# Kernel optimization log

Hardware: AMD Instinct MI355X
Metric: run time of the kernel (lower is better)

## Reference

```python
import jax, jax.numpy as jnp
import numpy as np

B, L, D = 32, 128, 512
Qn = 16          # n_querys
N, P = 512, 64   # gathered groups x group size


def setup_inputs() -> dict:
    key = jax.random.key(0)
    ks = jax.random.split(key, 10)
    s = 0.02
    return {
        "patch": jax.random.normal(ks[0], (B, L, D), jnp.float32),
        "query": jax.random.normal(ks[1], (1, Qn, D), jnp.float32),
        "Wk": jax.random.normal(ks[2], (D, D), jnp.float32) * s,
        "bk": jnp.zeros((D,), jnp.float32),
        "Wv": jax.random.normal(ks[3], (D, D), jnp.float32) * s,
        "bv": jnp.zeros((D,), jnp.float32),
        "Wf": jax.random.normal(ks[4], (D, 1), jnp.float32) * s,
        "bf": jnp.zeros((1,), jnp.float32),
        "indices": jax.random.randint(ks[5], (N, P), 0, B * L),
        "pos_mask": jax.random.bernoulli(ks[6], 0.8, (N, P)),
    }


def reference(patch, query, Wk, bk, Wv, bv, Wf, bf, indices, pos_mask):
    # patch: [B,L,D]; query: [1,q,D]; indices: [N,P] into B*L; pos_mask: [N,P]
    b, l, d = patch.shape
    q = query.shape[1]
    scale = 1.0 / jnp.sqrt(jnp.asarray(d, patch.dtype))
    Q0 = query[0]                                   # [q,D]
    # Projections (proj_k/proj_v applied to [Q ; patch]); Q row identical across batch
    KQ = Q0 @ Wk + bk                               # [q,D]
    Kp = patch @ Wk + bk                            # [B,L,D]
    VQ = Q0 @ Wv + bv                               # [q,D]
    Vp = patch @ Wv + bv                            # [B,L,D]
    # attn scores: self-token column (same for every batch) + patch columns
    s_self = jnp.einsum('qd,qd->q', Q0, KQ) * scale            # [q]
    s_patch = jnp.einsum('qd,bld->blq', Q0, Kp) * scale        # [B,L,q]
    # gather groups of tokens by flat index
    g = s_patch.reshape(b * l, q)[indices]                     # [N,P,q]
    g = jnp.where(pos_mask[:, :, None], g, -jnp.inf)
    g = jnp.transpose(g, (0, 2, 1))                            # [N,q,P]
    scores = jnp.concatenate(
        [jnp.broadcast_to(s_self[None, :, None], (g.shape[0], q, 1)), g], axis=-1)
    w = jax.nn.softmax(scores, axis=-1)                        # [N,q,P+1]
    # gathered values (value of a token is independent of q in the original)
    Vg = Vp.reshape(b * l, d)[indices]                         # [N,P,D]
    Vg = jnp.where(pos_mask[:, :, None], Vg, 0.0)
    patch_token = w[:, :, 0:1] * VQ[None] \
        + jnp.einsum('nqp,npd->nqd', w[:, :, 1:], Vg)          # [N,q,D]
    # fusion attention pooling over the q query axis
    fw = jax.nn.softmax(jnp.einsum('nqd,do->nqo', patch_token, Wf) + bf, axis=1)
    return jnp.sum(patch_token * fw, axis=1)                   # [N,D]
```

## Files before the change

kernel.cpp:

```cpp
#include <hip/hip_runtime.h>
#include <hip/hip_bf16.h>
#include <math.h>

#define DD    512
#define QN    16
#define NTOK  4096
#define MEXT  4112
#define MPAD  4224
#define NGRP  512
#define PP    64
#define NB    576
#define SCALE 0.04419417382415922f

typedef __bf16 bf16x8 __attribute__((ext_vector_type(8)));
typedef float  f32x4  __attribute__((ext_vector_type(4)));

static __device__ __forceinline__ ushort f2bf(float f) {
    __hip_bfloat16 h = __float2bfloat16(f);
    return *reinterpret_cast<ushort*>(&h);
}
static __device__ __forceinline__ float2 bfp2f2(unsigned int v) {
    float2 r;
    r.x = __uint_as_float(v << 16);
    r.y = __uint_as_float(v & 0xffff0000u);
    return r;
}
static __device__ __forceinline__ void gload16(const void* g, void* l) {
    __builtin_amdgcn_global_load_lds(
        (const __attribute__((address_space(1))) void*)g,
        (__attribute__((address_space(3))) void*)l, 16, 0, 0);
}

__global__ __launch_bounds__(256) void pack_all(
    const float* __restrict__ patch, const float* __restrict__ query,
    const float* __restrict__ Wv, const float* __restrict__ Wk,
    const float* __restrict__ bk,
    ushort* __restrict__ Xb, ushort* __restrict__ Bb, float* __restrict__ c0)
{
    __shared__ float T[64][65];
    const int b = blockIdx.x;
    const int tid = threadIdx.x;
    if (b < 1056) {
        const int e0 = b * 2048 + tid * 8;
        const int row = e0 >> 9, c = e0 & 511;
        float v[8];
        if (row < NTOK) {
            const float4 a0 = *(const float4*)&patch[(size_t)row * DD + c];
            const float4 a1 = *(const float4*)&patch[(size_t)row * DD + c + 4];
            v[0]=a0.x; v[1]=a0.y; v[2]=a0.z; v[3]=a0.w;
            v[4]=a1.x; v[5]=a1.y; v[6]=a1.z; v[7]=a1.w;
        } else if (row < MEXT) {
            const float4 a0 = *(const float4*)&query[(size_t)(row - NTOK) * DD + c];
            const float4 a1 = *(const float4*)&query[(size_t)(row - NTOK) * DD + c + 4];
            v[0]=a0.x; v[1]=a0.y; v[2]=a0.z; v[3]=a0.w;
            v[4]=a1.x; v[5]=a1.y; v[6]=a1.z; v[7]=a1.w;
        } else {
#pragma unroll
            for (int j = 0; j < 8; ++j) v[j] = 0.f;
        }
        ushort o[8];
#pragma unroll
        for (int j = 0; j < 8; ++j) o[j] = f2bf(v[j]);
        *(uint4*)&Xb[e0] = *(const uint4*)o;
    } else if (b < 1120) {
        const int t = b - 1056;
        const int k0 = (t >> 3) * 64, n0 = (t & 7) * 64;
#pragma unroll
        for (int j = 0; j < 16; ++j) {
            const int idx = tid + j * 256;
            const int r = idx >> 6, c = idx & 63;
            T[r][c] = Wv[(size_t)(k0 + r) * DD + n0 + c];
        }
        __syncthreads();
#pragma unroll
        for (int j = 0; j < 16; ++j) {
            const int idx = tid + j * 256;
            const int r = idx >> 6, c = idx & 63;
            Bb[(size_t)(n0 + r) * DD + k0 + c] = f2bf(T[c][r]);
        }
    } else if (b < 1132) {
        const int e0 = (b - 1120) * 2048 + tid * 8;
        *(uint4*)&Bb[(size_t)528 * DD + e0] = make_uint4(0, 0, 0, 0);
    } else {
        const int wave = tid >> 6, lane = tid & 63;
        const int g = (b - 1132) * 4 + wave;
        if (g < DD) {
            const int e = g;
            float x[8];
#pragma unroll
            for (int j = 0; j < 8; ++j) x[j] = Wk[e * DD + j * 64 + lane];
            for (int q = 0; q < QN; ++q) {
                float s = 0.f;
#pragma unroll
                for (int j = 0; j < 8; ++j) s += x[j] * query[q * DD + j * 64 + lane];
#pragma unroll
                for (int off = 32; off > 0; off >>= 1) s += __shfl_down(s, off, 64);
                if (lane == 0) Bb[(size_t)(DD + q) * DD + e] = f2bf(s);
            }
        } else {
            const int q = g - DD;
            float s = 0.f;
#pragma unroll
            for (int j = 0; j < 8; ++j)
                s += bk[j * 64 + lane] * query[q * DD + j * 64 + lane];
#pragma unroll
            for (int off = 32; off > 0; off >>= 1) s += __shfl_down(s, off, 64);
            if (lane == 0) c0[q] = s;
        }
    }
}

__global__ __launch_bounds__(256) void k2_mfma(
    const ushort* __restrict__ Xb, const ushort* __restrict__ Bb,
    const float* __restrict__ bv, const float* __restrict__ c0,
    ushort* __restrict__ VpH, float* __restrict__ S)
{
    __shared__ __align__(16) ushort Xs[64 * 64];
    __shared__ __align__(16) ushort Bs[64 * 64];
    const int tid = threadIdx.x;
    const int rowBase = blockIdx.y * 64;
    const int colBase = blockIdx.x * 64;
    const int wave = tid >> 6, lane = tid & 63;
    const int wm = (wave >> 1) * 32, wn = (wave & 1) * 32;
    const int lr = lane & 15;
    const int quad = lane >> 4;

    f32x4 acc[2][2];
    const f32x4 zero = {0.f, 0.f, 0.f, 0.f};
#pragma unroll
    for (int i = 0; i < 2; ++i) { acc[i][0] = zero; acc[i][1] = zero; }

    char* XsB = (char*)Xs;
    char* BsB = (char*)Bs;

    for (int k0 = 0; k0 < DD; k0 += 64) {
#pragma unroll
        for (int i = 0; i < 2; ++i) {
            const int L = i * 4096 + tid * 16;
            const int r = L >> 7;
            const int cB = (L & 127) ^ ((r & 7) << 4);
            gload16((const char*)&Xb[(size_t)(rowBase + r) * DD + k0] + cB, XsB + L);
            gload16((const char*)&Bb[(size_t)(colBase + r) * DD + k0] + cB, BsB + L);
        }
        __syncthreads();
#pragma unroll
        for (int kc = 0; kc < 2; ++kc) {
            bf16x8 af[2], bfr[2];
#pragma unroll
            for (int t = 0; t < 2; ++t) {
                const int ar = wm + t * 16 + lr;
                const int ab = (ar * 128 + kc * 64 + quad * 16) ^ ((ar & 7) << 4);
                af[t] = *(const bf16x8*)(XsB + ab);
            }
#pragma unroll
            for (int u = 0; u < 2; ++u) {
                const int br = wn + u * 16 + lr;
                const int bb = (br * 128 + kc * 64 + quad * 16) ^ ((br & 7) << 4);
                bfr[u] = *(const bf16x8*)(BsB + bb);
            }
#pragma unroll
            for (int mt = 0; mt < 2; ++mt)
#pragma unroll
                for (int nt = 0; nt < 2; ++nt)
                    acc[mt][nt] = __builtin_amdgcn_mfma_f32_16x16x32_bf16(
                        af[mt], bfr[nt], acc[mt][nt], 0, 0, 0);
        }
        __syncthreads();
    }

#pragma unroll
    for (int nt = 0; nt < 2; ++nt) {
        const int col = colBase + wn + nt * 16 + lr;
        const bool isV = (col < DD);
        const bool isS = (col >= DD) && (col < DD + QN);
        const float badd = isV ? bv[col] : (isS ? c0[col - DD] : 0.f);
#pragma unroll
        for (int mt = 0; mt < 2; ++mt) {
#pragma unroll
            for (int r = 0; r < 4; ++r) {
                const int row = rowBase + wm + mt * 16 + quad * 4 + r;
                if (row < MEXT) {
                    const float v = acc[mt][nt][r];
                    if (isV)      VpH[(size_t)row * DD + col] = f2bf(v + badd);
                    else if (isS) S[row * QN + (col - DD)] = (v + badd) * SCALE;
                }
            }
        }
    }
}

__global__ __launch_bounds__(256) void k4_agg(
    const ushort* __restrict__ VpH,
    const float* __restrict__ S,
    const int* __restrict__ indices,
    const void* __restrict__ pmask,
    const float* __restrict__ Wf, const float* __restrict__ bf,
    float* __restrict__ out)
{
    __shared__ int   idxs[PP];
    __shared__ int   mval[PP];
    __shared__ int   cidx[PP + 8];
    __shared__ int   cp[PP + 8];
    __shared__ float scT[PP + 2][QN];
    __shared__ float red[QN][4];
    __shared__ float fwq[QN];
    __shared__ int   cntS;

    const int n = blockIdx.x;
    const int tid = threadIdx.x;

    const unsigned int* mw = (const unsigned int*)pmask;
    bool four = true;
#pragma unroll
    for (int i = 0; i < 16; ++i) {
        const unsigned int v = mw[i];
        four = four && (v == 0u || v == 1u || v == 0x3F800000u);
    }

    if (tid < PP) {
        idxs[tid] = indices[n * PP + tid];
        int mv;
        if (four) mv = (mw[n * PP + tid] != 0u);
        else      mv = (((const unsigned char*)pmask)[n * PP + tid] != 0);
        mval[tid] = mv;
        const bool a = (mv != 0);
        const unsigned long long m = __ballot(a);
        const int pos = __popcll(m & ((1ull << tid) - 1ull));
        if (a) { cidx[pos] = idxs[tid]; cp[pos] = tid; }
        if (tid == 0) cntS = (int)__popcll(m);
    }
    __syncthreads();

    for (int e = tid; e < QN * PP; e += 256) {
        const int p = e >> 4, q = e & 15;
        scT[p + 1][q] = mval[p] ? S[idxs[p] * QN + q] : -INFINITY;
    }
    if (tid < QN) scT[0][tid] = S[(NTOK + tid) * QN + tid];
    __syncthreads();

    if (tid < 8) { cidx[cntS + tid] = 0; cp[cntS + tid] = PP; }
    if (tid < QN) {
        const int q = tid;
        float m = -INFINITY;
        for (int j = 0; j <= PP; ++j) m = fmaxf(m, scT[j][q]);
        float s = 0.f;
        for (int j = 0; j <= PP; ++j) { const float e = __expf(scT[j][q] - m); scT[j][q] = e; s += e; }
        const float inv = 1.f / s;
        for (int j = 0; j <= PP; ++j) scT[j][q] *= inv;
        scT[PP + 1][q] = 0.f;
    }
    __syncthreads();

    const int cnt8 = (cntS + 7) & ~7;
    const int d0 = tid * 2;
    float pt[QN][2];
    {
        float2 vq[QN];
#pragma unroll
        for (int q = 0; q < QN; ++q)
            vq[q] = bfp2f2(*(const unsigned int*)&VpH[(size_t)(NTOK + q) * DD + d0]);
#pragma unroll
        for (int q = 0; q < QN; ++q) {
            const float w0 = scT[0][q];
            pt[q][0] = w0 * vq[q].x;
            pt[q][1] = w0 * vq[q].y;
        }
    }
    for (int j0 = 0; j0 < cnt8; j0 += 8) {
        float2 v[8]; int p[8];
#pragma unroll
        for (int pi = 0; pi < 8; ++pi) {
            v[pi] = bfp2f2(*(const unsigned int*)&VpH[(size_t)cidx[j0 + pi] * DD + d0]);
            p[pi] = cp[j0 + pi] + 1;
        }
#pragma unroll
        for (int pi = 0; pi < 8; ++pi) {
            const float4 wa = *(const float4*)&scT[p[pi]][0];
            const float4 wb = *(const float4*)&scT[p[pi]][4];
            const float4 wc = *(const float4*)&scT[p[pi]][8];
            const float4 wd = *(const float4*)&scT[p[pi]][12];
            const float vx = v[pi].x, vy = v[pi].y;
            pt[ 0][0] += wa.x*vx; pt[ 0][1] += wa.x*vy;
            pt[ 1][0] += wa.y*vx; pt[ 1][1] += wa.y*vy;
            pt[ 2][0] += wa.z*vx; pt[ 2][1] += wa.z*vy;
            pt[ 3][0] += wa.w*vx; pt[ 3][1] += wa.w*vy;
            pt[ 4][0] += wb.x*vx; pt[ 4][1] += wb.x*vy;
            pt[ 5][0] += wb.y*vx; pt[ 5][1] += wb.y*vy;
            pt[ 6][0] += wb.z*vx; pt[ 6][1] += wb.z*vy;
            pt[ 7][0] += wb.w*vx; pt[ 7][1] += wb.w*vy;
            pt[ 8][0] += wc.x*vx; pt[ 8][1] += wc.x*vy;
            pt[ 9][0] += wc.y*vx; pt[ 9][1] += wc.y*vy;
            pt[10][0] += wc.z*vx; pt[10][1] += wc.z*vy;
            pt[11][0] += wc.w*vx; pt[11][1] += wc.w*vy;
            pt[12][0] += wd.x*vx; pt[12][1] += wd.x*vy;
            pt[13][0] += wd.y*vx; pt[13][1] += wd.y*vy;
            pt[14][0] += wd.z*vx; pt[14][1] += wd.z*vy;
            pt[15][0] += wd.w*vx; pt[15][1] += wd.w*vy;
        }
    }

    const float wf0 = Wf[d0], wf1 = Wf[d0 + 1];
    const int wid = tid >> 6, lane = tid & 63;
#pragma unroll
    for (int q = 0; q < QN; ++q) {
        float s = pt[q][0] * wf0 + pt[q][1] * wf1;
#pragma unroll
        for (int off = 32; off > 0; off >>= 1) s += __shfl_down(s, off, 64);
        if (lane == 0) red[q][wid] = s;
    }
    __syncthreads();
    if (tid == 0) {
        float f[QN];
        float m = -INFINITY;
#pragma unroll
        for (int q = 0; q < QN; ++q) {
            f[q] = red[q][0] + red[q][1] + red[q][2] + red[q][3] + bf[0];
            m = fmaxf(m, f[q]);
        }
        float ssum = 0.f;
#pragma unroll
        for (int q = 0; q < QN; ++q) { f[q] = __expf(f[q] - m); ssum += f[q]; }
        const float inv = 1.f / ssum;
#pragma unroll
        for (int q = 0; q < QN; ++q) fwq[q] = f[q] * inv;
    }
    __syncthreads();

    float o0 = 0.f, o1 = 0.f;
#pragma unroll
    for (int q = 0; q < QN; ++q) {
        const float w = fwq[q];
        o0 += pt[q][0] * w;
        o1 += pt[q][1] * w;
    }
    *(float2*)&out[(size_t)n * DD + d0] = make_float2(o0, o1);
}

extern "C" void kernel_launch(void* const* d_in, const int* in_sizes, int n_in,
                              void* d_out, int out_size, void* d_ws, size_t ws_size,
                              hipStream_t stream)
{
    const float* patch   = (const float*)d_in[0];
    const float* query   = (const float*)d_in[1];
    const float* Wk      = (const float*)d_in[2];
    const float* bk      = (const float*)d_in[3];
    const float* Wv      = (const float*)d_in[4];
    const float* bv      = (const float*)d_in[5];
    const float* Wf      = (const float*)d_in[6];
    const float* bf      = (const float*)d_in[7];
    const int*   indices = (const int*)d_in[8];
    const void*  pmask   = d_in[9];
    float* out = (float*)d_out;

    ushort* VpH = (ushort*)d_ws;
    float*  S   = (float*)(VpH + (size_t)MEXT * DD);
    float*  c0  = S + (size_t)MEXT * QN;
    ushort* Xb  = (ushort*)(c0 + 16);
    ushort* Bb  = Xb + (size_t)MPAD * DD;

    pack_all<<<dim3(1264), dim3(256), 0, stream>>>(patch, query, Wv, Wk, bk, Xb, Bb, c0);
    k2_mfma <<<dim3(9, 66), dim3(256), 0, stream>>>(Xb, Bb, bv, c0, VpH, S);
    k4_agg  <<<dim3(NGRP), dim3(256), 0, stream>>>(VpH, S, indices, pmask, Wf, bf, out);
}
```

Before: 118.9 us.

## Fuse fp32-to-bf16 patch conversion into GEMM and double-buffer LDS tiles

Result: slower. 121.8 us (+2.4%).

```diff
diff --git a/kernel.cpp b/kernel.cpp
--- a/kernel.cpp
+++ b/kernel.cpp
@@ -6,7 +6,6 @@
 #define QN    16
 #define NTOK  4096
 #define MEXT  4112
-#define MPAD  4224
 #define NGRP  512
 #define PP    64
 #define NB    576
@@ -30,41 +29,24 @@
         (const __attribute__((address_space(1))) void*)g,
         (__attribute__((address_space(3))) void*)l, 16, 0, 0);
 }
-
-__global__ __launch_bounds__(256) void pack_all(
-    const float* __restrict__ patch, const float* __restrict__ query,
+static __device__ __forceinline__ void packstore(char* dst, float4 a, float4 b) {
+    ushort o[8];
+    o[0]=f2bf(a.x); o[1]=f2bf(a.y); o[2]=f2bf(a.z); o[3]=f2bf(a.w);
+    o[4]=f2bf(b.x); o[5]=f2bf(b.y); o[6]=f2bf(b.z); o[7]=f2bf(b.w);
+    *(uint4*)dst = *(const uint4*)o;
+}
+
+__global__ __launch_bounds__(256) void pack_b(
+    const float* __restrict__ query,
     const float* __restrict__ Wv, const float* __restrict__ Wk,
     const float* __restrict__ bk,
-    ushort* __restrict__ Xb, ushort* __restrict__ Bb, float* __restrict__ c0)
+    ushort* __restrict__ Bb, float* __restrict__ c0, float* __restrict__ xtail)
 {
     __shared__ float T[64][65];
     const int b = blockIdx.x;
     const int tid = threadIdx.x;
-    if (b < 1056) {
-        const int e0 = b * 2048 + tid * 8;
-        const int row = e0 >> 9, c = e0 & 511;
-        float v[8];
-        if (row < NTOK) {
-            const float4 a0 = *(const float4*)&patch[(size_t)row * DD + c];
-            const float4 a1 = *(const float4*)&patch[(size_t)row * DD + c + 4];
-            v[0]=a0.x; v[1]=a0.y; v[2]=a0.z; v[3]=a0.w;
-            v[4]=a1.x; v[5]=a1.y; v[6]=a1.z; v[7]=a1.w;
-        } else if (row < MEXT) {
-            const float4 a0 = *(const float4*)&query[(size_t)(row - NTOK) * DD + c];
-            const float4 a1 = *(const float4*)&query[(size_t)(row - NTOK) * DD + c + 4];
-            v[0]=a0.x; v[1]=a0.y; v[2]=a0.z; v[3]=a0.w;
-            v[4]=a1.x; v[5]=a1.y; v[6]=a1.z; v[7]=a1.w;
-        } else {
-#pragma unroll
-            for (int j = 0; j < 8; ++j) v[j] = 0.f;
-        }
-        ushort o[8];
-#pragma unroll
-        for (int j = 0; j < 8; ++j) o[j] = f2bf(v[j]);
-        *(uint4*)&Xb[e0] = *(const uint4*)o;
-    } else if (b < 1120) {
-        const int t = b - 1056;
-        const int k0 = (t >> 3) * 64, n0 = (t & 7) * 64;
+    if (b < 64) {
+        const int k0 = (b >> 3) * 64, n0 = (b & 7) * 64;
 #pragma unroll
         for (int j = 0; j < 16; ++j) {
             const int idx = tid + j * 256;
@@ -78,12 +60,12 @@
             const int r = idx >> 6, c = idx & 63;
             Bb[(size_t)(n0 + r) * DD + k0 + c] = f2bf(T[c][r]);
         }
-    } else if (b < 1132) {
-        const int e0 = (b - 1120) * 2048 + tid * 8;
+    } else if (b < 76) {
+        const int e0 = (b - 64) * 2048 + tid * 8;
         *(uint4*)&Bb[(size_t)528 * DD + e0] = make_uint4(0, 0, 0, 0);
-    } else {
+    } else if (b < 208) {
         const int wave = tid >> 6, lane = tid & 63;
-        const int g = (b - 1132) * 4 + wave;
+        const int g = (b - 76) * 4 + wave;
         if (g < DD) {
             const int e = g;
             float x[8];
@@ -97,7 +79,7 @@
                 for (int off = 32; off > 0; off >>= 1) s += __shfl_down(s, off, 64);
                 if (lane == 0) Bb[(size_t)(DD + q) * DD + e] = f2bf(s);
             }
-        } else {
+        } else if (g < DD + QN) {
             const int q = g - DD;
             float s = 0.f;
 #pragma unroll
@@ -107,16 +89,27 @@
             for (int off = 32; off > 0; off >>= 1) s += __shfl_down(s, off, 64);
             if (lane == 0) c0[q] = s;
         }
+    } else {
+        const int e0 = (b - 208) * 2048 + tid * 8;
+        const int row = e0 >> 9, c = e0 & 511;
+        float4 v0 = make_float4(0.f, 0.f, 0.f, 0.f), v1 = v0;
+        if (row < QN) {
+            v0 = *(const float4*)&query[(size_t)row * DD + c];
+            v1 = *(const float4*)&query[(size_t)row * DD + c + 4];
+        }
+        *(float4*)&xtail[e0]     = v0;
+        *(float4*)&xtail[e0 + 4] = v1;
     }
 }
 
 __global__ __launch_bounds__(256) void k2_mfma(
-    const ushort* __restrict__ Xb, const ushort* __restrict__ Bb,
+    const float* __restrict__ patch, const float* __restrict__ xtail,
+    const ushort* __restrict__ Bb,
     const float* __restrict__ bv, const float* __restrict__ c0,
     ushort* __restrict__ VpH, float* __restrict__ S)
 {
-    __shared__ __align__(16) ushort Xs[64 * 64];
-    __shared__ __align__(16) ushort Bs[64 * 64];
+    __shared__ __align__(16) ushort Xs[2][4096];
+    __shared__ __align__(16) ushort Bs[2][4096];
     const int tid = threadIdx.x;
     const int rowBase = blockIdx.y * 64;
     const int colBase = blockIdx.x * 64;
@@ -125,38 +118,66 @@
     const int lr = lane & 15;
     const int quad = lane >> 4;
 
+    const int r0 = tid >> 3;
+    const int r1 = r0 + 32;
+    const int c8 = (tid & 7) * 8;
+    const int row0 = rowBase + r0, row1 = rowBase + r1;
+    const float* s0 = ((row0 < NTOK) ? &patch[(size_t)row0 * DD]
+                                     : &xtail[(size_t)(row0 - NTOK) * DD]) + c8;
+    const float* s1 = ((row1 < NTOK) ? &patch[(size_t)row1 * DD]
+                                     : &xtail[(size_t)(row1 - NTOK) * DD]) + c8;
+    const int xw0 = (r0 * 128 + c8 * 2) ^ ((r0 & 7) << 4);
+    const int xw1 = (r1 * 128 + c8 * 2) ^ ((r1 & 7) << 4);
+
+    const int L0 = tid * 16;
+    const int L1 = 4096 + tid * 16;
+    const int br0 = L0 >> 7, bc0 = (L0 & 127) ^ ((br0 & 7) << 4);
+    const int br1 = L1 >> 7, bc1 = (L1 & 127) ^ ((br1 & 7) << 4);
+    const char* bsrc0 = (const char*)&Bb[(size_t)(colBase + br0) * DD] + bc0;
+    const char* bsrc1 = (const char*)&Bb[(size_t)(colBase + br1) * DD] + bc1;
+
+    char* XsB = (char*)Xs;
+    char* BsB = (char*)Bs;
+
     f32x4 acc[2][2];
     const f32x4 zero = {0.f, 0.f, 0.f, 0.f};
 #pragma unroll
     for (int i = 0; i < 2; ++i) { acc[i][0] = zero; acc[i][1] = zero; }
 
-    char* XsB = (char*)Xs;
-    char* BsB = (char*)Bs;
-
-    for (int k0 = 0; k0 < DD; k0 += 64) {
-#pragma unroll
-        for (int i = 0; i < 2; ++i) {
-            const int L = i * 4096 + tid * 16;
-            const int r = L >> 7;
-            const int cB = (L & 127) ^ ((r & 7) << 4);
-            gload16((const char*)&Xb[(size_t)(rowBase + r) * DD + k0] + cB, XsB + L);
-            gload16((const char*)&Bb[(size_t)(colBase + r) * DD + k0] + cB, BsB + L);
-        }
-        __syncthreads();
+    float4 xa, xb, xc, xd;
+    xa = *(const float4*)s0; xb = *(const float4*)(s0 + 4);
+    xc = *(const float4*)s1; xd = *(const float4*)(s1 + 4);
+    gload16(bsrc0, BsB + L0);
+    gload16(bsrc1, BsB + L1);
+    packstore(XsB + xw0, xa, xb);
+    packstore(XsB + xw1, xc, xd);
+    __syncthreads();
+
+#pragma unroll
+    for (int t = 0; t < 8; ++t) {
+        const int buf = t & 1, nxt = buf ^ 1;
+        const int kf = (t + 1) * 64;
+        if (t < 7) {
+            xa = *(const float4*)(s0 + kf); xb = *(const float4*)(s0 + kf + 4);
+            xc = *(const float4*)(s1 + kf); xd = *(const float4*)(s1 + kf + 4);
+            gload16(bsrc0 + kf * 2, BsB + nxt * 8192 + L0);
+            gload16(bsrc1 + kf * 2, BsB + nxt * 8192 + L1);
+        }
+        const int BF = buf * 8192;
 #pragma unroll
         for (int kc = 0; kc < 2; ++kc) {
             bf16x8 af[2], bfr[2];
 #pragma unroll
-            for (int t = 0; t < 2; ++t) {
-                const int ar = wm + t * 16 + lr;
+            for (int m = 0; m < 2; ++m) {
+                const int ar = wm + m * 16 + lr;
                 const int ab = (ar * 128 + kc * 64 + quad * 16) ^ ((ar & 7) << 4);
-                af[t] = *(const bf16x8*)(XsB + ab);
+                af[m] = *(const bf16x8*)(XsB + BF + ab);
             }
 #pragma unroll
             for (int u = 0; u < 2; ++u) {
                 const int br = wn + u * 16 + lr;
                 const int bb = (br * 128 + kc * 64 + quad * 16) ^ ((br & 7) << 4);
-                bfr[u] = *(const bf16x8*)(BsB + bb);
+                bfr[u] = *(const bf16x8*)(BsB + BF + bb);
             }
 #pragma unroll
             for (int mt = 0; mt < 2; ++mt)
@@ -164,6 +185,10 @@
                 for (int nt = 0; nt < 2; ++nt)
                     acc[mt][nt] = __builtin_amdgcn_mfma_f32_16x16x32_bf16(
                         af[mt], bfr[nt], acc[mt][nt], 0, 0, 0);
+        }
+        if (t < 7) {
+            packstore(XsB + nxt * 8192 + xw0, xa, xb);
+            packstore(XsB + nxt * 8192 + xw1, xc, xd);
         }
         __syncthreads();
     }
@@ -352,13 +377,13 @@
     const void*  pmask   = d_in[9];
     float* out = (float*)d_out;
 
-    ushort* VpH = (ushort*)d_ws;
-    float*  S   = (float*)(VpH + (size_t)MEXT * DD);
-    float*  c0  = S + (size_t)MEXT * QN;
-    ushort* Xb  = (ushort*)(c0 + 16);
-    ushort* Bb  = Xb + (size_t)MPAD * DD;
-
-    pack_all<<<dim3(1264), dim3(256), 0, stream>>>(patch, query, Wv, Wk, bk, Xb, Bb, c0);
-    k2_mfma <<<dim3(9, 66), dim3(256), 0, stream>>>(Xb, Bb, bv, c0, VpH, S);
-    k4_agg  <<<dim3(NGRP), dim3(256), 0, stream>>>(VpH, S, indices, pmask, Wf, bf, out);
-}
+    ushort* VpH   = (ushort*)d_ws;
+    float*  S     = (float*)(VpH + (size_t)MEXT * DD);
+    float*  c0    = S + (size_t)MEXT * QN;
+    ushort* Bb    = (ushort*)(c0 + 16);
+    float*  xtail = (float*)(Bb + (size_t)NB * DD);
+
+    pack_b<<<dim3(240), dim3(256), 0, stream>>>(query, Wv, Wk, bk, Bb, c0, xtail);
+    k2_mfma<<<dim3(9, 66), dim3(256), 0, stream>>>(patch, xtail, Bb, bv, c0, VpH, S);
+    k4_agg <<<dim3(NGRP), dim3(256), 0, stream>>>(VpH, S, indices, pmask, Wf, bf, out);
+}
```
